# Kernel optimization log

Hardware: AMD Instinct MI355X
Metric: run time of the kernel (lower is better)

Reference implementation:

```python
import jax, jax.numpy as jnp
import numpy as np

G = 64; B = 4; PER = 25000; N = B * PER
C_SEM = 64; C_MOS = 64; C = 32; NCLS = 26
OFFS = [(dx, dy, dz) for dx in (-1, 0, 1) for dy in (-1, 0, 1) for dz in (-1, 0, 1)]  # 27 kernel offsets


def _build_sparse():
    """Random active voxels per batch + [N,27] submanifold neighbor map (-1 = absent)."""
    rng = np.random.default_rng(0)
    keys_l, coords_l = [], []
    for b in range(B):
        lin = np.sort(rng.choice(G ** 3, size=PER, replace=False))
        x, y, z = lin // (G * G), (lin // G) % G, lin % G
        coords_l.append(np.stack([np.full(PER, b), x, y, z], 1))
        keys_l.append(b * (G ** 3) + lin)
    keys = np.concatenate(keys_l)
    co = np.concatenate(coords_l)
    order = np.argsort(keys, kind='stable')
    sk = keys[order]
    nbr = np.full((N, 27), -1, np.int64)
    bx, x, y, z = co[:, 0], co[:, 1], co[:, 2], co[:, 3]
    for k, (dx, dy, dz) in enumerate(OFFS):
        nx, ny, nz = x + dx, y + dy, z + dz
        ok = (nx >= 0) & (nx < G) & (ny >= 0) & (ny < G) & (nz >= 0) & (nz < G)
        nk = bx * (G ** 3) + nx * (G * G) + ny * G + nz
        pos = np.clip(np.searchsorted(sk, nk), 0, N - 1)
        hit = ok & (sk[pos] == nk)
        nbr[:, k] = np.where(hit, order[pos], -1)
    return co[:, 0].astype(np.int32), nbr.astype(np.int32)


def setup_inputs() -> dict:
    key = jax.random.key(0)
    ks = jax.random.split(key, 16)
    bids, nbr = _build_sparse()
    nrm = lambda k, s: jax.random.normal(ks[k], s, jnp.float32) * 0.05
    return {
        'feat_sem': jax.random.normal(ks[0], (N, C_SEM), jnp.float32),
        'feat_mos': jax.random.normal(ks[1], (N, C_MOS), jnp.float32),
        'fus_sp_w': nrm(2, (C_MOS, 1)), 'fus_sp_b': jnp.zeros((1,), jnp.float32),
        'fus_ch_w': nrm(3, (C_SEM, C_SEM)), 'fus_ch_b': jnp.zeros((C_SEM,), jnp.float32),
        'conv_w': nrm(4, (27, C_SEM, C)), 'conv_b': jnp.zeros((C,), jnp.float32),
        'r1c1_w': nrm(5, (27, C, C)), 'r1g1': jnp.ones((C,), jnp.float32), 'r1b1': jnp.zeros((C,), jnp.float32),
        'r1c2_w': nrm(6, (27, C, C)), 'r1g2': jnp.ones((C,), jnp.float32), 'r1b2': jnp.zeros((C,), jnp.float32),
        'ca1_w': nrm(7, (C, C // 8)), 'ca2_w': nrm(8, (C // 8, C)),
        'r2c1_w': nrm(9, (27, C, C)), 'r2g1': jnp.ones((C,), jnp.float32), 'r2b1': jnp.zeros((C,), jnp.float32),
        'r2c2_w': nrm(10, (27, C, C)), 'r2g2': jnp.ones((C,), jnp.float32), 'r2b2': jnp.zeros((C,), jnp.float32),
        'out_g': jnp.ones((C,), jnp.float32), 'out_b': jnp.zeros((C,), jnp.float32),
        'lin_w': nrm(11, (C, NCLS)), 'lin_b': jnp.zeros((NCLS,), jnp.float32),
        'batch_ids': jnp.asarray(bids), 'nbr': jnp.asarray(nbr), 'num_batches': B,
    }


def _subm3(x, W, nbr, b=None):
    # x: [N,Cin], W: [27,Cin,Cout], nbr: [N,27] (-1 = missing neighbor)
    valid = nbr >= 0
    g = x[jnp.where(valid, nbr, 0)] * valid[..., None].astype(x.dtype)  # [N,27,Cin]
    out = jnp.einsum('nkc,kco->no', g, W)
    return out if b is None else out + b


def _bn(x, g, b, eps=1e-4):
    # BatchNorm1d in training mode: batch stats over N, biased variance
    m = jnp.mean(x, 0)
    v = jnp.mean((x - m) ** 2, 0)
    return (x - m) * jax.lax.rsqrt(v + eps) * g + b


def _seg_mean(x, ids, nb):
    s = jax.ops.segment_sum(x, ids, num_segments=nb)
    c = jax.ops.segment_sum(jnp.ones((x.shape[0], 1), x.dtype), ids, num_segments=nb)
    return s / c


def _forward(feat_sem, feat_mos, fus_sp_w, fus_sp_b, fus_ch_w, fus_ch_b, conv_w, conv_b,
             r1c1_w, r1g1, r1b1, r1c2_w, r1g2, r1b2, ca1_w, ca2_w,
             r2c1_w, r2g1, r2b1, r2c2_w, r2g2, r2b2, out_g, out_b, lin_w, lin_b,
             batch_ids, nbr, num_batches):
    # ---- fusion_module_MGA_3D ----
    fm = jax.nn.sigmoid(feat_mos @ fus_sp_w + fus_sp_b) * feat_sem        # [N,Csem]
    vec = _seg_mean(fm, batch_ids, num_batches) @ fus_ch_w + fus_ch_b    # [B,Csem]
    vec = jax.nn.softmax(vec, axis=1) * vec.shape[1]
    fm = fm * vec[batch_ids]
    feat = fm + feat_sem
    # ---- conv ----
    h = _subm3(feat, conv_w, nbr, conv_b)                                # [N,32]

    def resblock(h, c1w, g1, b1, c2w, g2, b2):
        o = jax.nn.relu(_bn(_subm3(h, c1w, nbr), g1, b1))
        o = _bn(_subm3(o, c2w, nbr), g2, b2)
        return jax.nn.relu(o + h)

    h = resblock(h, r1c1_w, r1g1, r1b1, r1c2_w, r1g2, r1b2)
    # ---- ChannelAttention3D ----
    avg = _seg_mean(h, batch_ids, num_batches)
    mx = jax.ops.segment_max(h, batch_ids, num_segments=num_batches)
    mlp = lambda v: jax.nn.relu(v @ ca1_w) @ ca2_w
    att = jax.nn.sigmoid(mlp(avg) + mlp(mx))                             # [B,32]
    h = h * att[batch_ids]
    h = resblock(h, r2c1_w, r2g1, r2b1, r2c2_w, r2g2, r2b2)
    # ---- output layer ----
    h = jax.nn.relu(_bn(h, out_g, out_b))
    return h @ lin_w + lin_b                                             # [N,NCLS]


def reference(feat_sem, feat_mos, fus_sp_w, fus_sp_b, fus_ch_w, fus_ch_b, conv_w, conv_b,
              r1c1_w, r1g1, r1b1, r1c2_w, r1g2, r1b2, ca1_w, ca2_w,
              r2c1_w, r2g1, r2b1, r2c2_w, r2g2, r2b2, out_g, out_b, lin_w, lin_b,
              batch_ids, nbr, num_batches):
    return _forward(feat_sem, feat_mos, fus_sp_w, fus_sp_b, fus_ch_w, fus_ch_b, conv_w, conv_b,
                    r1c1_w, r1g1, r1b1, r1c2_w, r1g2, r1b2, ca1_w, ca2_w,
                    r2c1_w, r2g1, r2b1, r2c2_w, r2g2, r2b2, out_g, out_b, lin_w, lin_b,
                    batch_ids, nbr, num_batches)
```

## Files before the change

### kernel.cpp

```cpp
#include <hip/hip_runtime.h>
#include <math.h>

#define BMAX 4
typedef __attribute__((ext_vector_type(8))) short s16x8;
typedef __attribute__((ext_vector_type(4))) float f32x4;

__device__ __forceinline__ float sigmoidf_(float x) { return 1.f / (1.f + expf(-x)); }

__device__ __forceinline__ ushort f2b(float f) {
    uint u = __float_as_uint(f);
    u = u + 0x7FFFu + ((u >> 16) & 1u);
    return (ushort)(u >> 16);
}
__device__ __forceinline__ uint pk2(float a, float b) {
    return (uint)f2b(a) | ((uint)f2b(b) << 16);
}

__global__ __launch_bounds__(256)
void k_fuse_s(const float* __restrict__ mos, const float* __restrict__ spw,
              const float* __restrict__ spb, const int* __restrict__ bids,
              float* __restrict__ s_out, float* __restrict__ pc, int N)
{
    __shared__ float lcnt[BMAX];
    int tid = threadIdx.x;
    if (tid < BMAX) lcnt[tid] = 0.f;
    __syncthreads();
    int n = blockIdx.x * 256 + tid;
    if (n < N) {
        const float* mr = mos + (size_t)n * 64;
        float dot = 0.f;
        #pragma unroll
        for (int c = 0; c < 64; c += 4) {
            float4 m4 = *(const float4*)(mr + c);
            float4 w4 = *(const float4*)(spw + c);
            dot += m4.x * w4.x + m4.y * w4.y + m4.z * w4.z + m4.w * w4.w;
        }
        float s = sigmoidf_(dot + spb[0]);
        s_out[n] = s;
        atomicAdd(&lcnt[bids[n]], 1.f);
    }
    __syncthreads();
    if (tid < BMAX) pc[(size_t)blockIdx.x * 4 + tid] = lcnt[tid];
}

__global__ __launch_bounds__(256)
void k_seg_part(const float* __restrict__ fsem, const float* __restrict__ s_buf,
                const int* __restrict__ bids, float* __restrict__ part, int N)
{
    __shared__ float lseg[BMAX * 64];
    int tid = threadIdx.x;
    lseg[tid] = 0.f;
    __syncthreads();
    int c = tid & 63;
    int slot = blockIdx.x * 4 + (tid >> 6);
    int nslots = gridDim.x * 4;
    int chunk = (N + nslots - 1) / nslots;
    int n0 = slot * chunk;
    int n1 = min(N, n0 + chunk);
    float acc = 0.f; int curb = -1;
    int n = n0;
    for (; n + 4 <= n1; n += 4) {
        int b0 = bids[n], b3 = bids[n + 3];
        float s0 = s_buf[n], s1 = s_buf[n + 1], s2 = s_buf[n + 2], s3 = s_buf[n + 3];
        float f0 = fsem[(size_t)n * 64 + c];
        float f1 = fsem[(size_t)(n + 1) * 64 + c];
        float f2 = fsem[(size_t)(n + 2) * 64 + c];
        float f3 = fsem[(size_t)(n + 3) * 64 + c];
        if (b0 == b3) {
            if (b0 != curb) {
                if (curb >= 0) atomicAdd(&lseg[curb * 64 + c], acc);
                acc = 0.f; curb = b0;
            }
            acc += s0 * f0 + s1 * f1 + s2 * f2 + s3 * f3;
        } else {
            int bb[4] = { b0, bids[n + 1], bids[n + 2], b3 };
            float sv[4] = { s0, s1, s2, s3 };
            float fv[4] = { f0, f1, f2, f3 };
            #pragma unroll
            for (int q = 0; q < 4; ++q) {
                if (bb[q] != curb) {
                    if (curb >= 0) atomicAdd(&lseg[curb * 64 + c], acc);
                    acc = 0.f; curb = bb[q];
                }
                acc += sv[q] * fv[q];
            }
        }
    }
    for (; n < n1; ++n) {
        int b = bids[n];
        if (b != curb) {
            if (curb >= 0) atomicAdd(&lseg[curb * 64 + c], acc);
            acc = 0.f; curb = b;
        }
        acc += s_buf[n] * fsem[(size_t)n * 64 + c];
    }
    if (curb >= 0) atomicAdd(&lseg[curb * 64 + c], acc);
    __syncthreads();
    part[(size_t)blockIdx.x * 256 + tid] = lseg[tid];
}

__global__ __launch_bounds__(1024)
void k_seg_red(const float* __restrict__ part, float* __restrict__ seg, int nblk)
{
    __shared__ float l[1024];
    int tid = threadIdx.x;
    int col = tid & 255, grp = tid >> 8;
    float a = 0.f;
    #pragma unroll 8
    for (int j = grp; j < nblk; j += 4) a += part[(size_t)j * 256 + col];
    l[tid] = a;
    __syncthreads();
    if (tid < 256) seg[tid] = l[tid] + l[256 + tid] + l[512 + tid] + l[768 + tid];
}

__global__ void k_vec(const float* __restrict__ seg, const float* __restrict__ pc, int nbc,
                      const float* __restrict__ chw, const float* __restrict__ chb,
                      float* __restrict__ vec, float* __restrict__ cnt_out)
{
    __shared__ float lred[256];
    __shared__ float lcnt[4];
    int tid = threadIdx.x;
    float a = 0.f;
    for (int j = tid >> 2; j < nbc; j += 64) a += pc[(size_t)j * 4 + (tid & 3)];
    lred[tid] = a;
    __syncthreads();
    if (tid < 4) {
        float s = 0.f;
        #pragma unroll 8
        for (int j = 0; j < 64; ++j) s += lred[j * 4 + tid];
        lcnt[tid] = s;
        cnt_out[tid] = s;
    }
    __syncthreads();
    int b = tid >> 6;
    int c = tid & 63;
    float mean = seg[b * 64 + c] / lcnt[b];
    float v = chb[c];
    #pragma unroll 1
    for (int i = 0; i < 64; ++i) {
        float mi = __shfl(mean, i, 64);
        v += mi * chw[i * 64 + c];
    }
    float m = v;
    #pragma unroll
    for (int off = 32; off; off >>= 1) m = fmaxf(m, __shfl_xor(m, off, 64));
    float e = expf(v - m);
    float ssum = e;
    #pragma unroll
    for (int off = 32; off; off >>= 1) ssum += __shfl_xor(ssum, off, 64);
    vec[b * 64 + c] = e / ssum * 64.f;
}

__global__ __launch_bounds__(256)
void k_gate_cvt(const float* __restrict__ fs, const float* __restrict__ s_buf,
                const float* __restrict__ vec, const int* __restrict__ bids,
                ushort* __restrict__ out, int N)
{
    int n = blockIdx.x * 256 + threadIdx.x;
    if (n >= N) return;
    float s = s_buf[n];
    const float* vr = vec + bids[n] * 64;
    const float* fr = fs + (size_t)n * 64;
    ushort* orow = out + (size_t)n * 64;
    #pragma unroll
    for (int c = 0; c < 64; c += 8) {
        float4 f0 = *(const float4*)(fr + c);
        float4 f1 = *(const float4*)(fr + c + 4);
        float4 v0 = *(const float4*)(vr + c);
        float4 v1 = *(const float4*)(vr + c + 4);
        float g0 = f0.x * (1.f + s * v0.x), g1 = f0.y * (1.f + s * v0.y);
        float g2 = f0.z * (1.f + s * v0.z), g3 = f0.w * (1.f + s * v0.w);
        float g4 = f1.x * (1.f + s * v1.x), g5 = f1.y * (1.f + s * v1.y);
        float g6 = f1.z * (1.f + s * v1.z), g7 = f1.w * (1.f + s * v1.w);
        uint4 o; o.x = pk2(g0, g1); o.y = pk2(g2, g3); o.z = pk2(g4, g5); o.w = pk2(g6, g7);
        *(uint4*)(orow + c) = o;
    }
}

__device__ __forceinline__ void wpack_one(const float* __restrict__ W, int CIN,
                                          int tt, ushort* __restrict__ dst)
{
    int nkc = CIN >> 5;
    int lane = tt & 63;
    int nt = (tt >> 6) & 1;
    int kc = (tt >> 7) % nkc;
    int k = tt / (nkc * 128);
    int kk = kc * 32 + (lane >> 4) * 8;
    int col = nt * 16 + (lane & 15);
    const float* src = W + ((size_t)k * CIN + kk) * 32 + col;
    float v[8];
    #pragma unroll
    for (int e = 0; e < 8; ++e) v[e] = src[e * 32];
    uint4 o; o.x = pk2(v[0], v[1]); o.y = pk2(v[2], v[3]);
    o.z = pk2(v[4], v[5]); o.w = pk2(v[6], v[7]);
    *(uint4*)(dst + (size_t)tt * 8) = o;
}

__global__ __launch_bounds__(256)
void k_wpack_all(const float* __restrict__ W0, const float* __restrict__ W1,
                 const float* __restrict__ W2, const float* __restrict__ W3,
                 const float* __restrict__ W4, ushort* __restrict__ P)
{
    int t = blockIdx.x * 256 + threadIdx.x;
    if (t < 6912) {
        wpack_one(W0, 64, t, P);
    } else {
        int r = t - 6912;
        int s = r / 3456;
        int tt = r % 3456;
        if (s >= 4) return;
        const float* W = (s == 0) ? W1 : (s == 1) ? W2 : (s == 2) ? W3 : W4;
        wpack_one(W, 32, tt, P + 55296 + s * 27648);
    }
}

template<int CIN, bool STATS, bool BIAS, bool WB16>
__global__ __launch_bounds__(256)
void k_mconv(const ushort* __restrict__ inb, const int* __restrict__ nbr,
             const ushort* __restrict__ wpk, const float* __restrict__ bias,
             float* __restrict__ outf, ushort* __restrict__ outb,
             float* __restrict__ pp, int N)
{
    __shared__ float lsum[32];
    __shared__ float lsq[32];
    int tid = threadIdx.x;
    if (STATS) {
        if (tid < 32) { lsum[tid] = 0.f; lsq[tid] = 0.f; }
        __syncthreads();
    }
    int lane = tid & 63;
    int gw = (blockIdx.x * 256 + tid) >> 6;
    int vbase = gw * 32;
    bool wact = vbase < N;
    float ps0 = 0.f, pq0 = 0.f, ps1 = 0.f, pq1 = 0.f;
    if (wact) {
        int row = lane & 15;
        int koff = (lane >> 4) * 8;
        f32x4 acc00 = {0.f,0.f,0.f,0.f}, acc01 = {0.f,0.f,0.f,0.f};
        f32x4 acc10 = {0.f,0.f,0.f,0.f}, acc11 = {0.f,0.f,0.f,0.f};
        const int* nb0 = nbr + (size_t)(vbase + row) * 27;
        const int* nb1 = nbr + (size_t)(vbase + 16 + row) * 27;
        #pragma unroll
        for (int k = 0; k < 27; ++k) {
            int j0 = nb0[k];
            int j1 = nb1[k];
            #pragma unroll
            for (int kc = 0; kc < CIN / 32; ++kc) {
                s16x8 a0 = {0,0,0,0,0,0,0,0};
                s16x8 a1 = {0,0,0,0,0,0,0,0};
                if (j0 >= 0) a0 = *(const s16x8*)(inb + (size_t)j0 * CIN + kc * 32 + koff);
                if (j1 >= 0) a1 = *(const s16x8*)(inb + (size_t)j1 * CIN + kc * 32 + koff);
                const ushort* wb = wpk + (size_t)(k * (CIN / 32) + kc) * 1024 + lane * 8;
                s16x8 b0 = *(const s16x8*)(wb);
                s16x8 b1 = *(const s16x8*)(wb + 512);
                acc00 = __builtin_amdgcn_mfma_f32_16x16x32_bf16(a0, b0, acc00, 0, 0, 0);
                acc01 = __builtin_amdgcn_mfma_f32_16x16x32_bf16(a0, b1, acc01, 0, 0, 0);
                acc10 = __builtin_amdgcn_mfma_f32_16x16x32_bf16(a1, b0, acc10, 0, 0, 0);
                acc11 = __builtin_amdgcn_mfma_f32_16x16x32_bf16(a1, b1, acc11, 0, 0, 0);
            }
        }
        int ccol = lane & 15;
        int crow = (lane >> 4) * 4;
        float b0v = BIAS ? bias[ccol] : 0.f;
        float b1v = BIAS ? bias[16 + ccol] : 0.f;
        #pragma unroll
        for (int mt = 0; mt < 2; ++mt) {
            const f32x4& A0 = mt ? acc10 : acc00;
            const f32x4& A1 = mt ? acc11 : acc01;
            #pragma unroll
            for (int i = 0; i < 4; ++i) {
                int v = vbase + mt * 16 + crow + i;
                float x0 = A0[i] + b0v;
                float x1 = A1[i] + b1v;
                outf[(size_t)v * 32 + ccol] = x0;
                outf[(size_t)v * 32 + 16 + ccol] = x1;
                if (WB16) {
                    outb[(size_t)v * 32 + ccol] = f2b(x0);
                    outb[(size_t)v * 32 + 16 + ccol] = f2b(x1);
                }
                if (STATS) { ps0 += x0; pq0 += x0 * x0; ps1 += x1; pq1 += x1 * x1; }
            }
        }
    }
    if (STATS) {
        ps0 += __shfl_xor(ps0, 16, 64); ps0 += __shfl_xor(ps0, 32, 64);
        pq0 += __shfl_xor(pq0, 16, 64); pq0 += __shfl_xor(pq0, 32, 64);
        ps1 += __shfl_xor(ps1, 16, 64); ps1 += __shfl_xor(ps1, 32, 64);
        pq1 += __shfl_xor(pq1, 16, 64); pq1 += __shfl_xor(pq1, 32, 64);
        if (lane < 16) {
            atomicAdd(&lsum[lane], ps0);
            atomicAdd(&lsq[lane], pq0);
            atomicAdd(&lsum[16 + lane], ps1);
            atomicAdd(&lsq[16 + lane], pq1);
        }
        __syncthreads();
        if (tid < 32) {
            pp[(size_t)blockIdx.x * 64 + tid] = lsum[tid];
            pp[(size_t)blockIdx.x * 64 + 32 + tid] = lsq[tid];
        }
    }
}

__global__ __launch_bounds__(1024)
void k_statsr(const float* __restrict__ part, int nblk,
              const float* __restrict__ g, const float* __restrict__ bb,
              float* __restrict__ sc, float* __restrict__ sh, float invN)
{
    __shared__ float l[1024];
    int tid = threadIdx.x;
    int col = tid & 63, grp = tid >> 6;
    float a = 0.f;
    #pragma unroll 8
    for (int j = grp; j < nblk; j += 16) a += part[(size_t)j * 64 + col];
    l[tid] = a;
    __syncthreads();
    if (tid < 64) {
        float s = 0.f;
        #pragma unroll
        for (int gq = 0; gq < 16; ++gq) s += l[gq * 64 + tid];
        l[tid] = s;
    }
    __syncthreads();
    if (tid < 32) {
        float m = l[tid] * invN;
        float v = l[32 + tid] * invN - m * m;
        float s = g[tid] * rsqrtf(v + 1e-4f);
        sc[tid] = s;
        sh[tid] = bb[tid] - m * s;
    }
}

__global__ __launch_bounds__(256)
void k_bnact(const float* __restrict__ t, const float* __restrict__ sc,
             const float* __restrict__ sh, ushort* __restrict__ out, int N)
{
    int n = blockIdx.x * 256 + threadIdx.x;
    if (n >= N) return;
    const float* tr = t + (size_t)n * 32;
    ushort* orow = out + (size_t)n * 32;
    #pragma unroll
    for (int c = 0; c < 32; c += 8) {
        float4 t0 = *(const float4*)(tr + c);
        float4 t1 = *(const float4*)(tr + c + 4);
        float g0 = fmaxf(t0.x * sc[c+0] + sh[c+0], 0.f);
        float g1 = fmaxf(t0.y * sc[c+1] + sh[c+1], 0.f);
        float g2 = fmaxf(t0.z * sc[c+2] + sh[c+2], 0.f);
        float g3 = fmaxf(t0.w * sc[c+3] + sh[c+3], 0.f);
        float g4 = fmaxf(t1.x * sc[c+4] + sh[c+4], 0.f);
        float g5 = fmaxf(t1.y * sc[c+5] + sh[c+5], 0.f);
        float g6 = fmaxf(t1.z * sc[c+6] + sh[c+6], 0.f);
        float g7 = fmaxf(t1.w * sc[c+7] + sh[c+7], 0.f);
        uint4 o; o.x = pk2(g0, g1); o.y = pk2(g2, g3); o.z = pk2(g4, g5); o.w = pk2(g6, g7);
        *(uint4*)(orow + c) = o;
    }
}

__global__ __launch_bounds__(256)
void k_comb1(const float* __restrict__ t, const float* __restrict__ res,
             const float* __restrict__ sc, const float* __restrict__ sh,
             const int* __restrict__ bids, float* __restrict__ hout,
             float* __restrict__ part, int N)
{
    __shared__ float lsum[BMAX * 32];
    __shared__ int   lmax[BMAX * 32];
    int tid = threadIdx.x;
    if (tid < BMAX * 32) { lsum[tid] = 0.f; lmax[tid] = 0; }
    __syncthreads();
    int gid = blockIdx.x * 256 + tid;
    int n = gid >> 2;
    int c0 = (gid & 3) * 8;
    if (n < N) {
        int b = bids[n];
        const float* tr = t + (size_t)n * 32 + c0;
        const float* rr = res + (size_t)n * 32 + c0;
        float4 t0 = *(const float4*)tr, t1 = *(const float4*)(tr + 4);
        float4 r0 = *(const float4*)rr, r1 = *(const float4*)(rr + 4);
        float v[8];
        v[0] = fmaxf(t0.x * sc[c0+0] + sh[c0+0] + r0.x, 0.f);
        v[1] = fmaxf(t0.y * sc[c0+1] + sh[c0+1] + r0.y, 0.f);
        v[2] = fmaxf(t0.z * sc[c0+2] + sh[c0+2] + r0.z, 0.f);
        v[3] = fmaxf(t0.w * sc[c0+3] + sh[c0+3] + r0.w, 0.f);
        v[4] = fmaxf(t1.x * sc[c0+4] + sh[c0+4] + r1.x, 0.f);
        v[5] = fmaxf(t1.y * sc[c0+5] + sh[c0+5] + r1.y, 0.f);
        v[6] = fmaxf(t1.z * sc[c0+6] + sh[c0+6] + r1.z, 0.f);
        v[7] = fmaxf(t1.w * sc[c0+7] + sh[c0+7] + r1.w, 0.f);
        float4 o0 = { v[0], v[1], v[2], v[3] };
        float4 o1 = { v[4], v[5], v[6], v[7] };
        *(float4*)(hout + (size_t)n * 32 + c0) = o0;
        *(float4*)(hout + (size_t)n * 32 + c0 + 4) = o1;
        int base = b * 32 + c0;
        #pragma unroll
        for (int i = 0; i < 8; ++i) {
            atomicAdd(&lsum[base + i], v[i]);
            atomicMax(&lmax[base + i], __float_as_int(v[i]));
        }
    }
    __syncthreads();
    if (tid < 128) part[(size_t)blockIdx.x * 256 + tid] = lsum[tid];
    else           part[(size_t)blockIdx.x * 256 + tid] = __int_as_float(lmax[tid - 128]);
}

__global__ __launch_bounds__(256)
void k_attred(const float* __restrict__ part, int nblk, float* __restrict__ out)
{
    int tid = threadIdx.x;
    int blk = blockIdx.x;
    if (tid < 128) {
        float a = 0.f;
        #pragma unroll 4
        for (int j = blk; j < nblk; j += 64) a += part[(size_t)j * 256 + tid];
        out[(size_t)blk * 256 + tid] = a;
    } else {
        float m = 0.f;
        #pragma unroll 4
        for (int j = blk; j < nblk; j += 64) m = fmaxf(m, part[(size_t)j * 256 + tid]);
        out[(size_t)blk * 256 + tid] = m;
    }
}

__global__ void k_att(const float* __restrict__ part2, const float* __restrict__ cnt,
                      const float* __restrict__ ca1, const float* __restrict__ ca2,
                      float* __restrict__ att)
{
    __shared__ float seg[256];
    int tid = threadIdx.x;
    if (tid < 128) {
        float a = 0.f;
        #pragma unroll 8
        for (int j = 0; j < 64; ++j) a += part2[j * 256 + tid];
        seg[tid] = a;
    } else {
        float m = 0.f;
        #pragma unroll 8
        for (int j = 0; j < 64; ++j) m = fmaxf(m, part2[j * 256 + tid]);
        seg[tid] = m;
    }
    __syncthreads();
    int b = tid >> 6;
    int lane = tid & 63;
    bool actc = lane < 32;
    int c = lane & 31;
    float avg = actc ? seg[b * 32 + c] / cnt[b] : 0.f;
    float mx  = actc ? seg[128 + b * 32 + c] : 0.f;
    float h[8];
    #pragma unroll
    for (int i = 0; i < 4; ++i) {
        float w = actc ? ca1[c * 4 + i] : 0.f;
        h[i] = avg * w;
        h[i + 4] = mx * w;
    }
    #pragma unroll
    for (int off = 32; off; off >>= 1) {
        #pragma unroll
        for (int i = 0; i < 8; ++i) h[i] += __shfl_xor(h[i], off, 64);
    }
    if (actc) {
        float o = 0.f;
        #pragma unroll
        for (int i = 0; i < 4; ++i)
            o += (fmaxf(h[i], 0.f) + fmaxf(h[i + 4], 0.f)) * ca2[i * 32 + c];
        att[b * 32 + c] = sigmoidf_(o);
    }
}

__global__ __launch_bounds__(256)
void k_scale_cvt(const float* __restrict__ h1, const float* __restrict__ att,
                 const int* __restrict__ bids, float* __restrict__ hatt,
                 ushort* __restrict__ hattb, int N)
{
    int n = blockIdx.x * 256 + threadIdx.x;
    if (n >= N) return;
    const float* hr = h1 + (size_t)n * 32;
    const float* ar = att + bids[n] * 32;
    float* of = hatt + (size_t)n * 32;
    ushort* ob = hattb + (size_t)n * 32;
    #pragma unroll
    for (int c = 0; c < 32; c += 8) {
        float4 h0 = *(const float4*)(hr + c);
        float4 h1v = *(const float4*)(hr + c + 4);
        float4 a0 = *(const float4*)(ar + c);
        float4 a1 = *(const float4*)(ar + c + 4);
        float g0 = h0.x * a0.x, g1 = h0.y * a0.y, g2 = h0.z * a0.z, g3 = h0.w * a0.w;
        float g4 = h1v.x * a1.x, g5 = h1v.y * a1.y, g6 = h1v.z * a1.z, g7 = h1v.w * a1.w;
        float4 w0; w0.x = g0; w0.y = g1; w0.z = g2; w0.w = g3;
        float4 w1; w1.x = g4; w1.y = g5; w1.z = g6; w1.w = g7;
        *(float4*)(of + c) = w0;
        *(float4*)(of + c + 4) = w1;
        uint4 o; o.x = pk2(g0, g1); o.y = pk2(g2, g3); o.z = pk2(g4, g5); o.w = pk2(g6, g7);
        *(uint4*)(ob + c) = o;
    }
}

__global__ __launch_bounds__(256)
void k_comb2(const float* __restrict__ t, const float* __restrict__ hres,
             const float* __restrict__ sc, const float* __restrict__ sh,
             float* __restrict__ hout, float* __restrict__ part, int N)
{
    __shared__ float lsum[32];
    __shared__ float lsq[32];
    int tid = threadIdx.x;
    if (tid < 32) { lsum[tid] = 0.f; lsq[tid] = 0.f; }
    __syncthreads();
    int gid = blockIdx.x * 256 + tid;
    int n = gid >> 2;
    int c0 = (gid & 3) * 8;
    if (n < N) {
        const float* tr = t + (size_t)n * 32 + c0;
        const float* hr = hres + (size_t)n * 32 + c0;
        float4 t0 = *(const float4*)tr, t1 = *(const float4*)(tr + 4);
        float4 h0 = *(const float4*)hr, h1 = *(const float4*)(hr + 4);
        float v[8];
        v[0] = fmaxf(t0.x * sc[c0+0] + sh[c0+0] + h0.x, 0.f);
        v[1] = fmaxf(t0.y * sc[c0+1] + sh[c0+1] + h0.y, 0.f);
        v[2] = fmaxf(t0.z * sc[c0+2] + sh[c0+2] + h0.z, 0.f);
        v[3] = fmaxf(t0.w * sc[c0+3] + sh[c0+3] + h0.w, 0.f);
        v[4] = fmaxf(t1.x * sc[c0+4] + sh[c0+4] + h1.x, 0.f);
        v[5] = fmaxf(t1.y * sc[c0+5] + sh[c0+5] + h1.y, 0.f);
        v[6] = fmaxf(t1.z * sc[c0+6] + sh[c0+6] + h1.z, 0.f);
        v[7] = fmaxf(t1.w * sc[c0+7] + sh[c0+7] + h1.w, 0.f);
        float4 o0 = { v[0], v[1], v[2], v[3] };
        float4 o1 = { v[4], v[5], v[6], v[7] };
        *(float4*)(hout + (size_t)n * 32 + c0) = o0;
        *(float4*)(hout + (size_t)n * 32 + c0 + 4) = o1;
        #pragma unroll
        for (int i = 0; i < 8; ++i) {
            atomicAdd(&lsum[c0 + i], v[i]);
            atomicAdd(&lsq[c0 + i], v[i] * v[i]);
        }
    }
    __syncthreads();
    if (tid < 32) {
        part[(size_t)blockIdx.x * 64 + tid] = lsum[tid];
        part[(size_t)blockIdx.x * 64 + 32 + tid] = lsq[tid];
    }
}

__global__ __launch_bounds__(256)
void k_final(const float* __restrict__ h2, const float* __restrict__ sc,
             const float* __restrict__ sh, const float* __restrict__ lw,
             const float* __restrict__ lb, float* __restrict__ out, int N)
{
    int n = blockIdx.x * 256 + threadIdx.x;
    if (n >= N) return;
    const float* hr = h2 + (size_t)n * 32;
    float acc[26];
    #pragma unroll
    for (int o = 0; o < 26; ++o) acc[o] = lb[o];
    #pragma unroll
    for (int c4 = 0; c4 < 32; c4 += 4) {
        float4 hv = *(const float4*)(hr + c4);
        float xs[4] = { hv.x, hv.y, hv.z, hv.w };
        #pragma unroll
        for (int cc = 0; cc < 4; ++cc) {
            int c = c4 + cc;
            float x = fmaxf(xs[cc] * sc[c] + sh[c], 0.f);
            const float* wr = lw + c * 26;
            #pragma unroll
            for (int o = 0; o < 26; ++o) acc[o] += x * wr[o];
        }
    }
    float* orow = out + (size_t)n * 26;
    #pragma unroll
    for (int o = 0; o < 26; ++o) orow[o] = acc[o];
}

extern "C" void kernel_launch(void* const* d_in, const int* in_sizes, int n_in,
                              void* d_out, int out_size, void* d_ws, size_t ws_size,
                              hipStream_t stream)
{
    const float* feat_sem = (const float*)d_in[0];
    const float* feat_mos = (const float*)d_in[1];
    const float* fus_sp_w = (const float*)d_in[2];
    const float* fus_sp_b = (const float*)d_in[3];
    const float* fus_ch_w = (const float*)d_in[4];
    const float* fus_ch_b = (const float*)d_in[5];
    const float* conv_w   = (const float*)d_in[6];
    const float* conv_b   = (const float*)d_in[7];
    const float* r1c1_w   = (const float*)d_in[8];
    const float* r1g1     = (const float*)d_in[9];
    const float* r1b1     = (const float*)d_in[10];
    const float* r1c2_w   = (const float*)d_in[11];
    const float* r1g2     = (const float*)d_in[12];
    const float* r1b2     = (const float*)d_in[13];
    const float* ca1_w    = (const float*)d_in[14];
    const float* ca2_w    = (const float*)d_in[15];
    const float* r2c1_w   = (const float*)d_in[16];
    const float* r2g1     = (const float*)d_in[17];
    const float* r2b1     = (const float*)d_in[18];
    const float* r2c2_w   = (const float*)d_in[19];
    const float* r2g2     = (const float*)d_in[20];
    const float* r2b2     = (const float*)d_in[21];
    const float* out_g    = (const float*)d_in[22];
    const float* out_b    = (const float*)d_in[23];
    const float* lin_w    = (const float*)d_in[24];
    const float* lin_b    = (const float*)d_in[25];
    const int*   bids     = (const int*)d_in[26];
    const int*   nbr      = (const int*)d_in[27];
    int N = in_sizes[0] / 64;

    float* ws = (float*)d_ws;
    float* S1 = ws;
    float* S2 = ws + (size_t)32 * N;
    float* S3 = ws + (size_t)64 * N;
    float* S4 = ws + (size_t)96 * N;
    ushort* BB1 = (ushort*)(ws + (size_t)128 * N);
    ushort* BB2 = (ushort*)(ws + (size_t)144 * N);
    float* sbuf = (float*)BB2;
    ushort* FGB = (ushort*)S3;
    float* segpart = S2;
    float* st = ws + (size_t)160 * N;
    float* seg_fm = st;
    float* cnt    = st + 256;
    float* vec    = st + 260;
    float* bnsc   = st + 516;
    float* bnsh   = st + 676;
    float* attbuf = st + 840;
    float* pcnt   = st + 2048;
    float* at2    = st + 4096;
    ushort* wpk0 = (ushort*)(st + 20480);
    ushort* wpk1 = wpk0 + 55296;
    ushort* wpk2 = wpk1 + 27648;
    ushort* wpk3 = wpk2 + 27648;
    ushort* wpk4 = wpk3 + 27648;

    int nb  = (N + 255) / 256;
    int nw  = (N + 127) / 128;
    int nb4 = (N + 63) / 64;
    const int NSEG = 512;
    float invN = 1.f / (float)N;

    k_wpack_all<<<81, 256, 0, stream>>>(conv_w, r1c1_w, r1c2_w, r2c1_w, r2c2_w, wpk0);

    k_fuse_s<<<nb, 256, 0, stream>>>(feat_mos, fus_sp_w, fus_sp_b, bids, sbuf, pcnt, N);
    k_seg_part<<<NSEG, 256, 0, stream>>>(feat_sem, sbuf, bids, segpart, N);
    k_seg_red<<<1, 1024, 0, stream>>>(segpart, seg_fm, NSEG);
    k_vec<<<1, 256, 0, stream>>>(seg_fm, pcnt, nb, fus_ch_w, fus_ch_b, vec, cnt);
    k_gate_cvt<<<nb, 256, 0, stream>>>(feat_sem, sbuf, vec, bids, FGB, N);

    k_mconv<64, false, true, true><<<nw, 256, 0, stream>>>(FGB, nbr, wpk0, conv_b,
        S1, BB1, nullptr, N);

    k_mconv<32, true, false, false><<<nw, 256, 0, stream>>>(BB1, nbr, wpk1, nullptr,
        S2, nullptr, S4, N);
    k_statsr<<<1, 1024, 0, stream>>>(S4, nw, r1g1, r1b1, bnsc + 0, bnsh + 0, invN);
    k_bnact<<<nb, 256, 0, stream>>>(S2, bnsc + 0, bnsh + 0, BB2, N);

    k_mconv<32, true, false, false><<<nw, 256, 0, stream>>>(BB2, nbr, wpk2, nullptr,
        S3, nullptr, S4, N);
    k_statsr<<<1, 1024, 0, stream>>>(S4, nw, r1g2, r1b2, bnsc + 32, bnsh + 32, invN);

    k_comb1<<<nb4, 256, 0, stream>>>(S3, S1, bnsc + 32, bnsh + 32, bids, S4, S2, N);
    k_attred<<<64, 256, 0, stream>>>(S2, nb4, at2);
    k_att<<<1, 256, 0, stream>>>(at2, cnt, ca1_w, ca2_w, attbuf);
    k_scale_cvt<<<nb, 256, 0, stream>>>(S4, attbuf, bids, S2, BB1, N);

    k_mconv<32, true, false, false><<<nw, 256, 0, stream>>>(BB1, nbr, wpk3, nullptr,
        S1, nullptr, S3, N);
    k_statsr<<<1, 1024, 0, stream>>>(S3, nw, r2g1, r2b1, bnsc + 64, bnsh + 64, invN);
    k_bnact<<<nb, 256, 0, stream>>>(S1, bnsc + 64, bnsh + 64, BB2, N);

    k_mconv<32, true, false, false><<<nw, 256, 0, stream>>>(BB2, nbr, wpk4, nullptr,
        S3, nullptr, S4, N);
    k_statsr<<<1, 1024, 0, stream>>>(S4, nw, r2g2, r2b2, bnsc + 96, bnsh + 96, invN);

    k_comb2<<<nb4, 256, 0, stream>>>(S3, S2, bnsc + 96, bnsh + 96, S1, S4, N);
    k_statsr<<<1, 1024, 0, stream>>>(S4, nb4, out_g, out_b, bnsc + 128, bnsh + 128, invN);

    k_final<<<nb, 256, 0, stream>>>(S1, bnsc + 128, bnsh + 128, lin_w, lin_b, (float*)d_out, N);
}
```

Before: 515.7 us.

## Transpose neighbor map, use zero sentinel row, shrink conv tiles, widen elementwise kernels

Adds a kernel that transposes the neighbor map to [27,N] so each conv wave reads neighbor indices coalesced and preloads all 27 up front. Missing neighbors now point at an appended zero row instead of a branch, which keeps the gather loads unconditional. Each conv wave handles 16 voxels instead of 32, doubling the wave count. The elementwise kernels (gate, bnact, scale) use several threads per row, and the workspace is compacted with in-place residual updates. The smaller tiles give up reuse of the weight fragments across voxels.

```diff
diff --git a/kernel.cpp b/kernel.cpp
--- a/kernel.cpp
+++ b/kernel.cpp
@@ -14,6 +14,23 @@
 }
 __device__ __forceinline__ uint pk2(float a, float b) {
     return (uint)f2b(a) | ((uint)f2b(b) << 16);
+}
+
+__global__ __launch_bounds__(256)
+void k_nbrT(const int* __restrict__ nbr, int* __restrict__ nbrT, int N)
+{
+    __shared__ int l[64 * 27];
+    int tid = threadIdx.x;
+    int n0 = blockIdx.x * 64;
+    int nrows = min(64, N - n0);
+    int tot = nrows * 27;
+    for (int t = tid; t < tot; t += 256) l[t] = nbr[(size_t)n0 * 27 + t];
+    __syncthreads();
+    int lane = tid & 63;
+    if (lane < nrows) {
+        for (int k = tid >> 6; k < 27; k += 4)
+            nbrT[(size_t)k * N + n0 + lane] = l[lane * 27 + k];
+    }
 }
 
 __global__ __launch_bounds__(256)
@@ -156,25 +173,22 @@
                 const float* __restrict__ vec, const int* __restrict__ bids,
                 ushort* __restrict__ out, int N)
 {
-    int n = blockIdx.x * 256 + threadIdx.x;
+    int gid = blockIdx.x * 256 + threadIdx.x;
+    if (gid < 64) out[(size_t)N * 64 + gid] = 0;
+    int n = gid >> 3;
     if (n >= N) return;
+    int c0 = (gid & 7) * 8;
     float s = s_buf[n];
-    const float* vr = vec + bids[n] * 64;
-    const float* fr = fs + (size_t)n * 64;
-    ushort* orow = out + (size_t)n * 64;
-    #pragma unroll
-    for (int c = 0; c < 64; c += 8) {
-        float4 f0 = *(const float4*)(fr + c);
-        float4 f1 = *(const float4*)(fr + c + 4);
-        float4 v0 = *(const float4*)(vr + c);
-        float4 v1 = *(const float4*)(vr + c + 4);
-        float g0 = f0.x * (1.f + s * v0.x), g1 = f0.y * (1.f + s * v0.y);
-        float g2 = f0.z * (1.f + s * v0.z), g3 = f0.w * (1.f + s * v0.w);
-        float g4 = f1.x * (1.f + s * v1.x), g5 = f1.y * (1.f + s * v1.y);
-        float g6 = f1.z * (1.f + s * v1.z), g7 = f1.w * (1.f + s * v1.w);
-        uint4 o; o.x = pk2(g0, g1); o.y = pk2(g2, g3); o.z = pk2(g4, g5); o.w = pk2(g6, g7);
-        *(uint4*)(orow + c) = o;
-    }
+    const float* vr = vec + bids[n] * 64 + c0;
+    const float* fr = fs + (size_t)n * 64 + c0;
+    float4 f0 = *(const float4*)fr, f1 = *(const float4*)(fr + 4);
+    float4 v0 = *(const float4*)vr, v1 = *(const float4*)(vr + 4);
+    float g0 = f0.x * (1.f + s * v0.x), g1 = f0.y * (1.f + s * v0.y);
+    float g2 = f0.z * (1.f + s * v0.z), g3 = f0.w * (1.f + s * v0.w);
+    float g4 = f1.x * (1.f + s * v1.x), g5 = f1.y * (1.f + s * v1.y);
+    float g6 = f1.z * (1.f + s * v1.z), g7 = f1.w * (1.f + s * v1.w);
+    uint4 o; o.x = pk2(g0, g1); o.y = pk2(g2, g3); o.z = pk2(g4, g5); o.w = pk2(g6, g7);
+    *(uint4*)(out + (size_t)n * 64 + c0) = o;
 }
 
 __device__ __forceinline__ void wpack_one(const float* __restrict__ W, int CIN,
@@ -216,7 +230,7 @@
 
 template<int CIN, bool STATS, bool BIAS, bool WB16>
 __global__ __launch_bounds__(256)
-void k_mconv(const ushort* __restrict__ inb, const int* __restrict__ nbr,
+void k_mconv(const ushort* __restrict__ inb, const int* __restrict__ nbrT,
              const ushort* __restrict__ wpk, const float* __restrict__ bias,
              float* __restrict__ outf, ushort* __restrict__ outb,
              float* __restrict__ pp, int N)
@@ -224,39 +238,35 @@
     __shared__ float lsum[32];
     __shared__ float lsq[32];
     int tid = threadIdx.x;
+    if (WB16 && blockIdx.x == 0 && tid < 32) outb[(size_t)N * 32 + tid] = 0;
     if (STATS) {
         if (tid < 32) { lsum[tid] = 0.f; lsq[tid] = 0.f; }
         __syncthreads();
     }
     int lane = tid & 63;
     int gw = (blockIdx.x * 256 + tid) >> 6;
-    int vbase = gw * 32;
-    bool wact = vbase < N;
+    int vbase = gw * 16;
     float ps0 = 0.f, pq0 = 0.f, ps1 = 0.f, pq1 = 0.f;
-    if (wact) {
+    if (vbase < N) {
         int row = lane & 15;
         int koff = (lane >> 4) * 8;
-        f32x4 acc00 = {0.f,0.f,0.f,0.f}, acc01 = {0.f,0.f,0.f,0.f};
-        f32x4 acc10 = {0.f,0.f,0.f,0.f}, acc11 = {0.f,0.f,0.f,0.f};
-        const int* nb0 = nbr + (size_t)(vbase + row) * 27;
-        const int* nb1 = nbr + (size_t)(vbase + 16 + row) * 27;
+        int vr = vbase + row; if (vr >= N) vr = N - 1;
+        f32x4 acc0 = {0.f,0.f,0.f,0.f}, acc1 = {0.f,0.f,0.f,0.f};
+        int j[27];
+        #pragma unroll
+        for (int k = 0; k < 27; ++k) j[k] = nbrT[(size_t)k * N + vr];
         #pragma unroll
         for (int k = 0; k < 27; ++k) {
-            int j0 = nb0[k];
-            int j1 = nb1[k];
+            int jj = (j[k] < 0) ? N : j[k];
+            const ushort* arow = inb + (size_t)jj * CIN + koff;
             #pragma unroll
             for (int kc = 0; kc < CIN / 32; ++kc) {
-                s16x8 a0 = {0,0,0,0,0,0,0,0};
-                s16x8 a1 = {0,0,0,0,0,0,0,0};
-                if (j0 >= 0) a0 = *(const s16x8*)(inb + (size_t)j0 * CIN + kc * 32 + koff);
-                if (j1 >= 0) a1 = *(const s16x8*)(inb + (size_t)j1 * CIN + kc * 32 + koff);
+                s16x8 a = *(const s16x8*)(arow + kc * 32);
                 const ushort* wb = wpk + (size_t)(k * (CIN / 32) + kc) * 1024 + lane * 8;
                 s16x8 b0 = *(const s16x8*)(wb);
                 s16x8 b1 = *(const s16x8*)(wb + 512);
-                acc00 = __builtin_amdgcn_mfma_f32_16x16x32_bf16(a0, b0, acc00, 0, 0, 0);
-                acc01 = __builtin_amdgcn_mfma_f32_16x16x32_bf16(a0, b1, acc01, 0, 0, 0);
-                acc10 = __builtin_amdgcn_mfma_f32_16x16x32_bf16(a1, b0, acc10, 0, 0, 0);
-                acc11 = __builtin_amdgcn_mfma_f32_16x16x32_bf16(a1, b1, acc11, 0, 0, 0);
+                acc0 = __builtin_amdgcn_mfma_f32_16x16x32_bf16(a, b0, acc0, 0, 0, 0);
+                acc1 = __builtin_amdgcn_mfma_f32_16x16x32_bf16(a, b1, acc1, 0, 0, 0);
             }
         }
         int ccol = lane & 15;
@@ -264,14 +274,11 @@
         float b0v = BIAS ? bias[ccol] : 0.f;
         float b1v = BIAS ? bias[16 + ccol] : 0.f;
         #pragma unroll
-        for (int mt = 0; mt < 2; ++mt) {
-            const f32x4& A0 = mt ? acc10 : acc00;
-            const f32x4& A1 = mt ? acc11 : acc01;
-            #pragma unroll
-            for (int i = 0; i < 4; ++i) {
-                int v = vbase + mt * 16 + crow + i;
-                float x0 = A0[i] + b0v;
-                float x1 = A1[i] + b1v;
+        for (int i = 0; i < 4; ++i) {
+            int v = vbase + crow + i;
+            if (v < N) {
+                float x0 = acc0[i] + b0v;
+                float x1 = acc1[i] + b1v;
                 outf[(size_t)v * 32 + ccol] = x0;
                 outf[(size_t)v * 32 + 16 + ccol] = x1;
                 if (WB16) {
@@ -334,32 +341,29 @@
 void k_bnact(const float* __restrict__ t, const float* __restrict__ sc,
              const float* __restrict__ sh, ushort* __restrict__ out, int N)
 {
-    int n = blockIdx.x * 256 + threadIdx.x;
+    int gid = blockIdx.x * 256 + threadIdx.x;
+    if (gid < 32) out[(size_t)N * 32 + gid] = 0;
+    int n = gid >> 2;
     if (n >= N) return;
-    const float* tr = t + (size_t)n * 32;
-    ushort* orow = out + (size_t)n * 32;
-    #pragma unroll
-    for (int c = 0; c < 32; c += 8) {
-        float4 t0 = *(const float4*)(tr + c);
-        float4 t1 = *(const float4*)(tr + c + 4);
-        float g0 = fmaxf(t0.x * sc[c+0] + sh[c+0], 0.f);
-        float g1 = fmaxf(t0.y * sc[c+1] + sh[c+1], 0.f);
-        float g2 = fmaxf(t0.z * sc[c+2] + sh[c+2], 0.f);
-        float g3 = fmaxf(t0.w * sc[c+3] + sh[c+3], 0.f);
-        float g4 = fmaxf(t1.x * sc[c+4] + sh[c+4], 0.f);
-        float g5 = fmaxf(t1.y * sc[c+5] + sh[c+5], 0.f);
-        float g6 = fmaxf(t1.z * sc[c+6] + sh[c+6], 0.f);
-        float g7 = fmaxf(t1.w * sc[c+7] + sh[c+7], 0.f);
-        uint4 o; o.x = pk2(g0, g1); o.y = pk2(g2, g3); o.z = pk2(g4, g5); o.w = pk2(g6, g7);
-        *(uint4*)(orow + c) = o;
-    }
-}
-
-__global__ __launch_bounds__(256)
-void k_comb1(const float* __restrict__ t, const float* __restrict__ res,
-             const float* __restrict__ sc, const float* __restrict__ sh,
-             const int* __restrict__ bids, float* __restrict__ hout,
-             float* __restrict__ part, int N)
+    int c0 = (gid & 3) * 8;
+    const float* tr = t + (size_t)n * 32 + c0;
+    float4 t0 = *(const float4*)tr, t1 = *(const float4*)(tr + 4);
+    float g0 = fmaxf(t0.x * sc[c0+0] + sh[c0+0], 0.f);
+    float g1 = fmaxf(t0.y * sc[c0+1] + sh[c0+1], 0.f);
+    float g2 = fmaxf(t0.z * sc[c0+2] + sh[c0+2], 0.f);
+    float g3 = fmaxf(t0.w * sc[c0+3] + sh[c0+3], 0.f);
+    float g4 = fmaxf(t1.x * sc[c0+4] + sh[c0+4], 0.f);
+    float g5 = fmaxf(t1.y * sc[c0+5] + sh[c0+5], 0.f);
+    float g6 = fmaxf(t1.z * sc[c0+6] + sh[c0+6], 0.f);
+    float g7 = fmaxf(t1.w * sc[c0+7] + sh[c0+7], 0.f);
+    uint4 o; o.x = pk2(g0, g1); o.y = pk2(g2, g3); o.z = pk2(g4, g5); o.w = pk2(g6, g7);
+    *(uint4*)(out + (size_t)n * 32 + c0) = o;
+}
+
+__global__ __launch_bounds__(256)
+void k_comb1(const float* __restrict__ t, const float* __restrict__ sc,
+             const float* __restrict__ sh, const int* __restrict__ bids,
+             float* hr, float* __restrict__ part, int N)
 {
     __shared__ float lsum[BMAX * 32];
     __shared__ int   lmax[BMAX * 32];
@@ -372,7 +376,7 @@
     if (n < N) {
         int b = bids[n];
         const float* tr = t + (size_t)n * 32 + c0;
-        const float* rr = res + (size_t)n * 32 + c0;
+        float* rr = hr + (size_t)n * 32 + c0;
         float4 t0 = *(const float4*)tr, t1 = *(const float4*)(tr + 4);
         float4 r0 = *(const float4*)rr, r1 = *(const float4*)(rr + 4);
         float v[8];
@@ -386,8 +390,8 @@
         v[7] = fmaxf(t1.w * sc[c0+7] + sh[c0+7] + r1.w, 0.f);
         float4 o0 = { v[0], v[1], v[2], v[3] };
         float4 o1 = { v[4], v[5], v[6], v[7] };
-        *(float4*)(hout + (size_t)n * 32 + c0) = o0;
-        *(float4*)(hout + (size_t)n * 32 + c0 + 4) = o1;
+        *(float4*)rr = o0;
+        *(float4*)(rr + 4) = o1;
         int base = b * 32 + c0;
         #pragma unroll
         for (int i = 0; i < 8; ++i) {
@@ -468,33 +472,28 @@
                  const int* __restrict__ bids, float* __restrict__ hatt,
                  ushort* __restrict__ hattb, int N)
 {
-    int n = blockIdx.x * 256 + threadIdx.x;
+    int gid = blockIdx.x * 256 + threadIdx.x;
+    if (gid < 32) hattb[(size_t)N * 32 + gid] = 0;
+    int n = gid >> 2;
     if (n >= N) return;
-    const float* hr = h1 + (size_t)n * 32;
-    const float* ar = att + bids[n] * 32;
-    float* of = hatt + (size_t)n * 32;
-    ushort* ob = hattb + (size_t)n * 32;
-    #pragma unroll
-    for (int c = 0; c < 32; c += 8) {
-        float4 h0 = *(const float4*)(hr + c);
-        float4 h1v = *(const float4*)(hr + c + 4);
-        float4 a0 = *(const float4*)(ar + c);
-        float4 a1 = *(const float4*)(ar + c + 4);
-        float g0 = h0.x * a0.x, g1 = h0.y * a0.y, g2 = h0.z * a0.z, g3 = h0.w * a0.w;
-        float g4 = h1v.x * a1.x, g5 = h1v.y * a1.y, g6 = h1v.z * a1.z, g7 = h1v.w * a1.w;
-        float4 w0; w0.x = g0; w0.y = g1; w0.z = g2; w0.w = g3;
-        float4 w1; w1.x = g4; w1.y = g5; w1.z = g6; w1.w = g7;
-        *(float4*)(of + c) = w0;
-        *(float4*)(of + c + 4) = w1;
-        uint4 o; o.x = pk2(g0, g1); o.y = pk2(g2, g3); o.z = pk2(g4, g5); o.w = pk2(g6, g7);
-        *(uint4*)(ob + c) = o;
-    }
-}
-
-__global__ __launch_bounds__(256)
-void k_comb2(const float* __restrict__ t, const float* __restrict__ hres,
-             const float* __restrict__ sc, const float* __restrict__ sh,
-             float* __restrict__ hout, float* __restrict__ part, int N)
+    int c0 = (gid & 3) * 8;
+    const float* hrp = h1 + (size_t)n * 32 + c0;
+    const float* ar = att + bids[n] * 32 + c0;
+    float4 h0 = *(const float4*)hrp, h1v = *(const float4*)(hrp + 4);
+    float4 a0 = *(const float4*)ar, a1 = *(const float4*)(ar + 4);
+    float g0 = h0.x * a0.x, g1 = h0.y * a0.y, g2 = h0.z * a0.z, g3 = h0.w * a0.w;
+    float g4 = h1v.x * a1.x, g5 = h1v.y * a1.y, g6 = h1v.z * a1.z, g7 = h1v.w * a1.w;
+    float4 w0 = { g0, g1, g2, g3 };
+    float4 w1 = { g4, g5, g6, g7 };
+    *(float4*)(hatt + (size_t)n * 32 + c0) = w0;
+    *(float4*)(hatt + (size_t)n * 32 + c0 + 4) = w1;
+    uint4 o; o.x = pk2(g0, g1); o.y = pk2(g2, g3); o.z = pk2(g4, g5); o.w = pk2(g6, g7);
+    *(uint4*)(hattb + (size_t)n * 32 + c0) = o;
+}
+
+__global__ __launch_bounds__(256)
+void k_comb2(const float* __restrict__ t, const float* __restrict__ sc,
+             const float* __restrict__ sh, float* hr, float* __restrict__ part, int N)
 {
     __shared__ float lsum[32];
     __shared__ float lsq[32];
@@ -506,9 +505,9 @@
     int c0 = (gid & 3) * 8;
     if (n < N) {
         const float* tr = t + (size_t)n * 32 + c0;
-        const float* hr = hres + (size_t)n * 32 + c0;
+        float* rr = hr + (size_t)n * 32 + c0;
         float4 t0 = *(const float4*)tr, t1 = *(const float4*)(tr + 4);
-        float4 h0 = *(const float4*)hr, h1 = *(const float4*)(hr + 4);
+        float4 h0 = *(const float4*)rr, h1 = *(const float4*)(rr + 4);
         float v[8];
         v[0] = fmaxf(t0.x * sc[c0+0] + sh[c0+0] + h0.x, 0.f);
         v[1] = fmaxf(t0.y * sc[c0+1] + sh[c0+1] + h0.y, 0.f);
@@ -520,8 +519,8 @@
         v[7] = fmaxf(t1.w * sc[c0+7] + sh[c0+7] + h1.w, 0.f);
         float4 o0 = { v[0], v[1], v[2], v[3] };
         float4 o1 = { v[4], v[5], v[6], v[7] };
-        *(float4*)(hout + (size_t)n * 32 + c0) = o0;
-        *(float4*)(hout + (size_t)n * 32 + c0 + 4) = o1;
+        *(float4*)rr = o0;
+        *(float4*)(rr + 4) = o1;
         #pragma unroll
         for (int i = 0; i < 8; ++i) {
             atomicAdd(&lsum[c0 + i], v[i]);
@@ -602,69 +601,73 @@
     float* S1 = ws;
     float* S2 = ws + (size_t)32 * N;
     float* S3 = ws + (size_t)64 * N;
-    float* S4 = ws + (size_t)96 * N;
-    ushort* BB1 = (ushort*)(ws + (size_t)128 * N);
-    ushort* BB2 = (ushort*)(ws + (size_t)144 * N);
-    float* sbuf = (float*)BB2;
+    ushort* BB1 = (ushort*)(ws + (size_t)96 * N + 32);
+    ushort* BB2 = BB1 + (size_t)32 * (N + 16);
+    float* sbuf = S2;
     ushort* FGB = (ushort*)S3;
-    float* segpart = S2;
-    float* st = ws + (size_t)160 * N;
+    float* segpart = S1;
+    float* st = ws + (size_t)128 * N + 1024;
     float* seg_fm = st;
     float* cnt    = st + 256;
     float* vec    = st + 260;
     float* bnsc   = st + 516;
     float* bnsh   = st + 676;
     float* attbuf = st + 840;
-    float* pcnt   = st + 2048;
-    float* at2    = st + 4096;
-    ushort* wpk0 = (ushort*)(st + 20480);
+    float* pcnt   = st + 1024;
+    float* ppbuf  = st + 4096;
+    float* partbuf= ppbuf + ((size_t)(N + 63) / 64) * 64 + 64;
+    float* at2    = partbuf + ((size_t)4 * N + 255) / 256 * 256 + 256;
+    ushort* wpk0  = (ushort*)(at2 + 16384);
     ushort* wpk1 = wpk0 + 55296;
     ushort* wpk2 = wpk1 + 27648;
     ushort* wpk3 = wpk2 + 27648;
     ushort* wpk4 = wpk3 + 27648;
+    int* nbrT = (int*)(wpk0 + 165888);
 
     int nb  = (N + 255) / 256;
-    int nw  = (N + 127) / 128;
-    int nb4 = (N + 63) / 64;
+    int nb4 = (4 * N + 255) / 256;
+    int nb8 = (8 * N + 255) / 256;
+    int nw  = (N + 63) / 64;
     const int NSEG = 512;
     float invN = 1.f / (float)N;
 
     k_wpack_all<<<81, 256, 0, stream>>>(conv_w, r1c1_w, r1c2_w, r2c1_w, r2c2_w, wpk0);
+    k_nbrT<<<nw, 256, 0, stream>>>(nbr, nbrT, N);
 
     k_fuse_s<<<nb, 256, 0, stream>>>(feat_mos, fus_sp_w, fus_sp_b, bids, sbuf, pcnt, N);
     k_seg_part<<<NSEG, 256, 0, stream>>>(feat_sem, sbuf, bids, segpart, N);
     k_seg_red<<<1, 1024, 0, stream>>>(segpart, seg_fm, NSEG);
     k_vec<<<1, 256, 0, stream>>>(seg_fm, pcnt, nb, fus_ch_w, fus_ch_b, vec, cnt);
-    k_gate_cvt<<<nb, 256, 0, stream>>>(feat_sem, sbuf, vec, bids, FGB, N);
-
-    k_mconv<64, false, true, true><<<nw, 256, 0, stream>>>(FGB, nbr, wpk0, conv_b,
+    k_gate_cvt<<<nb8, 256, 0, stream>>>(feat_sem, sbuf, vec, bids, FGB, N);
+
+    k_mconv<64, false, true, true><<<nw, 256, 0, stream>>>(FGB, nbrT, wpk0, conv_b,
         S1, BB1, nullptr, N);
 
-    k_mconv<32, true, false, false><<<nw, 256, 0, stream>>>(BB1, nbr, wpk1, nullptr,
-        S2, nullptr, S4, N);
-    k_statsr<<<1, 1024, 0, stream>>>(S4, nw, r1g1, r1b1, bnsc + 0, bnsh + 0, invN);
-    k_bnact<<<nb, 256, 0, stream>>>(S2, bnsc + 0, bnsh + 0, BB2, N);
-
-    k_mconv<32, true, false, false><<<nw, 256, 0, stream>>>(BB2, nbr, wpk2, nullptr,
-        S3, nullptr, S4, N);
-    k_statsr<<<1, 1024, 0, stream>>>(S4, nw, r1g2, r1b2, bnsc + 32, bnsh + 32, invN);
-
-    k_comb1<<<nb4, 256, 0, stream>>>(S3, S1, bnsc + 32, bnsh + 32, bids, S4, S2, N);
-    k_attred<<<64, 256, 0, stream>>>(S2, nb4, at2);
+    k_mconv<32, true, false, false><<<nw, 256, 0, stream>>>(BB1, nbrT, wpk1, nullptr,
+        S2, nullptr, ppbuf, N);
+    k_statsr<<<1, 1024, 0, stream>>>(ppbuf, nw, r1g1, r1b1, bnsc + 0, bnsh + 0, invN);
+    k_bnact<<<nb4, 256, 0, stream>>>(S2, bnsc + 0, bnsh + 0, BB2, N);
+
+    k_mconv<32, true, false, false><<<nw, 256, 0, stream>>>(BB2, nbrT, wpk2, nullptr,
+        S3, nullptr, ppbuf, N);
+    k_statsr<<<1, 1024, 0, stream>>>(ppbuf, nw, r1g2, r1b2, bnsc + 32, bnsh + 32, invN);
+
+    k_comb1<<<nb4, 256, 0, stream>>>(S3, bnsc + 32, bnsh + 32, bids, S1, partbuf, N);
+    k_attred<<<64, 256, 0, stream>>>(partbuf, nb4, at2);
     k_att<<<1, 256, 0, stream>>>(at2, cnt, ca1_w, ca2_w, attbuf);
-    k_scale_cvt<<<nb, 256, 0, stream>>>(S4, attbuf, bids, S2, BB1, N);
-
-    k_mconv<32, true, false, false><<<nw, 256, 0, stream>>>(BB1, nbr, wpk3, nullptr,
-        S1, nullptr, S3, N);
-    k_statsr<<<1, 1024, 0, stream>>>(S3, nw, r2g1, r2b1, bnsc + 64, bnsh + 64, invN);
-    k_bnact<<<nb, 256, 0, stream>>>(S1, bnsc + 64, bnsh + 64, BB2, N);
-
-    k_mconv<32, true, false, false><<<nw, 256, 0, stream>>>(BB2, nbr, wpk4, nullptr,
-        S3, nullptr, S4, N);
-    k_statsr<<<1, 1024, 0, stream>>>(S4, nw, r2g2, r2b2, bnsc + 96, bnsh + 96, invN);
-
-    k_comb2<<<nb4, 256, 0, stream>>>(S3, S2, bnsc + 96, bnsh + 96, S1, S4, N);
-    k_statsr<<<1, 1024, 0, stream>>>(S4, nb4, out_g, out_b, bnsc + 128, bnsh + 128, invN);
-
-    k_final<<<nb, 256, 0, stream>>>(S1, bnsc + 128, bnsh + 128, lin_w, lin_b, (float*)d_out, N);
-}
+    k_scale_cvt<<<nb4, 256, 0, stream>>>(S1, attbuf, bids, S2, BB1, N);
+
+    k_mconv<32, true, false, false><<<nw, 256, 0, stream>>>(BB1, nbrT, wpk3, nullptr,
+        S3, nullptr, ppbuf, N);
+    k_statsr<<<1, 1024, 0, stream>>>(ppbuf, nw, r2g1, r2b1, bnsc + 64, bnsh + 64, invN);
+    k_bnact<<<nb4, 256, 0, stream>>>(S3, bnsc + 64, bnsh + 64, BB2, N);
+
+    k_mconv<32, true, false, false><<<nw, 256, 0, stream>>>(BB2, nbrT, wpk4, nullptr,
+        S1, nullptr, ppbuf, N);
+    k_statsr<<<1, 1024, 0, stream>>>(ppbuf, nw, r2g2, r2b2, bnsc + 96, bnsh + 96, invN);
+
+    k_comb2<<<nb4, 256, 0, stream>>>(S1, bnsc + 96, bnsh + 96, S2, ppbuf, N);
+    k_statsr<<<1, 1024, 0, stream>>>(ppbuf, nb4, out_g, out_b, bnsc + 128, bnsh + 128, invN);
+
+    k_final<<<nb, 256, 0, stream>>>(S2, bnsc + 128, bnsh + 128, lin_w, lin_b, (float*)d_out, N);
+}
```

Result: faster. 491.6 us (-4.7%).
